# Kernel tuning notes

Measured on AMD Instinct MI355X. Metric: run time of the kernel, lower is better.

The kernel has to match this reference:

```python
import jax, jax.numpy as jnp
import numpy as np
import itertools

M_MODES = 16      # optical modes
N_PHOTONS = 8     # photons, input_state = [1]*8 + [0]*8
N_STATES = 12870  # C(16, 8) no-bunching output Fock states
OUT_SIZE = 128
BATCH = 8


def _random_unitary(key, m):
    kr, ki = jax.random.split(key)
    z = jax.random.normal(kr, (m, m)) + 1j * jax.random.normal(ki, (m, m))
    q, _ = jnp.linalg.qr(z)
    return q.astype(jnp.complex64)


def setup_inputs() -> dict:
    key = jax.random.key(0)
    ks = jax.random.split(key, 8)
    x = jax.random.normal(ks[0], (BATCH, M_MODES), dtype=jnp.float32)
    theta1 = jax.random.normal(ks[1], (M_MODES,), dtype=jnp.float32) * jnp.pi
    theta2 = jax.random.normal(ks[2], (M_MODES,), dtype=jnp.float32) * jnp.pi
    # fixed passive mixing unitaries (circuit structure constants)
    mix = jnp.stack([_random_unitary(jax.random.fold_in(ks[3], i), M_MODES) for i in range(4)])
    m_real = mix.real.astype(jnp.float32)
    m_imag = mix.imag.astype(jnp.float32)
    weight = jax.random.normal(ks[4], (N_STATES, OUT_SIZE), dtype=jnp.float32) * 0.02
    bias = jnp.zeros((OUT_SIZE,), dtype=jnp.float32)
    # no-bunching output Fock basis: all C(16,8) mode subsets (sorted rows)
    rows_idx = jnp.asarray(np.array(list(itertools.combinations(range(M_MODES), N_PHOTONS)), dtype=np.int32))
    return {"x": x, "theta1": theta1, "theta2": theta2, "m_real": m_real,
            "m_imag": m_imag, "weight": weight, "bias": bias, "rows_idx": rows_idx}


def reference(x, theta1, theta2, m_real, m_imag, weight, bias, rows_idx):
    n = N_PHOTONS
    M = (m_real + 1j * m_imag).astype(jnp.complex64)  # [4, m, m]
    # circuit unitary: U(x) = M3 . D(theta2) . M2 . D(x) . M1 . D(theta1) . M0
    A = M[1] @ (jnp.exp(1j * theta1)[:, None] * M[0])        # [m, m]
    B = M[3] @ (jnp.exp(1j * theta2)[:, None] * M[2])        # [m, m]
    U = jnp.einsum('pm,bm,mn->bpn', B, jnp.exp(1j * x), A)   # [b, m, m]
    # photons enter the first n modes -> keep those columns
    Uin = U[:, :, :n]                                        # [b, m, n]
    # Ryser's permanent formula over all 2^n column subsets
    sub = jnp.arange(2 ** n)
    masks = ((sub[:, None] >> jnp.arange(n)[None, :]) & 1).astype(jnp.float32)  # [2^n, n]
    popc = masks.sum(-1)
    signs = jnp.where((popc % 2) == 0, 1.0, -1.0) * ((-1.0) ** n)               # [2^n]
    # row partial sums for every mode and subset
    V = jnp.einsum('bmn,sn->bms', Uin, masks.astype(jnp.complex64))             # [b, m, 2^n]
    # product over the n rows of each output state (small fixed loop, not a data loop)
    acc = V[:, rows_idx[:, 0], :]                            # [b, states, 2^n]
    for i in range(1, n):
        acc = acc * V[:, rows_idx[:, i], :]
    amps = jnp.einsum('bks,s->bk', acc, signs.astype(jnp.complex64))            # [b, states]
    probs = amps.real ** 2 + amps.imag ** 2
    probs = probs / jnp.sum(probs, axis=-1, keepdims=True)   # renormalize over no-bunching subspace
    return probs @ weight + bias                             # linear output mapping
```

## Files before the change

### kernel.cpp

```cpp
#include <hip/hip_runtime.h>
#include <math.h>

#define NB 8
#define NM 16
#define NPH 8
#define NSTATES 12870
#define NSUB 256
#define OUTS 128
#define NTILES 824
#define NSLOTS (NTILES*16)
#define NSG 16
#define SPH 16
#define NTG 4
#define TILES_PER_TG 206
#define NGRID 512
#define SLOTS_P2 32
#define NP2 412

struct Tables {
  int binom[17][9];
  unsigned char cls_masks[256];
  int cls_off[10];
  int nt1[9], nt2[9];
  int tile_off[10];
};

constexpr int cpopc(int x){ int c=0; while(x){ c += x & 1; x >>= 1; } return c; }

constexpr Tables make_tables(){
  Tables t{};
  for (int n=0;n<=16;n++)
    for (int k=0;k<=8;k++){
      if (k==0) t.binom[n][k]=1;
      else if (n==0) t.binom[n][k]=0;
      else t.binom[n][k]=t.binom[n-1][k-1]+t.binom[n-1][k];
    }
  int idx=0;
  for (int p=0;p<=8;p++){
    t.cls_off[p]=idx;
    for (int m=0;m<256;m++) if (cpopc(m)==p) t.cls_masks[idx++]=(unsigned char)m;
  }
  t.cls_off[9]=idx;
  int toff=0;
  for (int c=0;c<=8;c++){
    int R=t.binom[8][c], C=t.binom[8][8-c];
    t.nt1[c]=(R+3)/4; t.nt2[c]=(C+3)/4;
    t.tile_off[c]=toff; toff += t.nt1[c]*t.nt2[c];
  }
  t.tile_off[9]=toff;
  return t;
}

constexpr Tables HTBL = make_tables();
static_assert(HTBL.tile_off[9]==NTILES, "tile count");
static_assert(HTBL.cls_off[9]==256, "mask count");
__device__ const Tables TBL = HTBL;

#define WS_TMAP   256
#define WS_BSUM2  53248
#define WS_POUT2  66560
#define WS_PART   1757184

__device__ __forceinline__ float2 cmul(float2 a, float2 b){
  return make_float2(fmaf(a.x,b.x,-(a.y*b.y)), fmaf(a.x,b.y, a.y*b.x));
}
__device__ __forceinline__ void cmac(float2& acc, float2 a, float2 b){
  acc.x = fmaf(a.x, b.x, acc.x); acc.x = fmaf(-a.y, b.y, acc.x);
  acc.y = fmaf(a.x, b.y, acc.y); acc.y = fmaf(a.y, b.x, acc.y);
}

__global__ __launch_bounds__(256) void k_p1(
    const float* __restrict__ x, const float* __restrict__ th1,
    const float* __restrict__ th2, const float* __restrict__ mr,
    const float* __restrict__ mi, const int* __restrict__ rows, char* ws)
{
  __shared__ float2 P[32][256];
  float2* __restrict__ part = (float2*)(ws + WS_PART);
  int tid = threadIdx.x;
  int blk = blockIdx.x;
  int b = blk >> 6, rest = blk & 63, sg = rest >> 2, tg = rest & 3;
  int sbase = sg * SPH;

  float2 (*T1)[NM]  = reinterpret_cast<float2(*)[NM]>(P[0]);
  float2 (*T2)[NM]  = reinterpret_cast<float2(*)[NM]>(P[1]);
  float2 (*Am)[NM]  = reinterpret_cast<float2(*)[NM]>(P[2]);
  float2 (*Bm)[NM]  = reinterpret_cast<float2(*)[NM]>(P[3]);
  float2 (*EA)[NPH] = reinterpret_cast<float2(*)[NPH]>(P[4]);
  float2* exP = P[4] + 128;
  float2 (*UinL)[NPH] = reinterpret_cast<float2(*)[NPH]>(P[5]);

  {
    int r = tid >> 4, cc = tid & 15;
    float sn, cs;
    sincosf(th1[r], &sn, &cs);
    float a = mr[0*256 + tid], bb = mi[0*256 + tid];
    T1[r][cc] = make_float2(cs*a - sn*bb, cs*bb + sn*a);
    sincosf(th2[r], &sn, &cs);
    float a2 = mr[2*256 + tid], b2 = mi[2*256 + tid];
    T2[r][cc] = make_float2(cs*a2 - sn*b2, cs*b2 + sn*a2);
    if (tid < NM){ float s2, c2; sincosf(x[b*NM + tid], &s2, &c2); exP[tid] = make_float2(c2, s2); }
  }
  __syncthreads();
  {
    int r = tid >> 4, cc = tid & 15;
    float2 accA = make_float2(0,0), accB = make_float2(0,0);
    for (int m=0;m<NM;m++){
      float2 m1 = make_float2(mr[1*256 + r*16+m], mi[1*256 + r*16+m]);
      cmac(accA, m1, T1[m][cc]);
      float2 m3 = make_float2(mr[3*256 + r*16+m], mi[3*256 + r*16+m]);
      cmac(accB, m3, T2[m][cc]);
    }
    Am[r][cc] = accA; Bm[r][cc] = accB;
  }
  __syncthreads();
  if (tid < NM*NPH){ int m = tid >> 3, n = tid & 7; EA[m][n] = cmul(exP[m], Am[m][n]); }
  __syncthreads();
  if (tid < NM*NPH){
    int p = tid >> 3, n = tid & 7;
    float2 acc = make_float2(0,0);
    for (int m=0;m<NM;m++) cmac(acc, Bm[p][m], EA[m][n]);
    UinL[p][n] = acc;
  }
  __syncthreads();

  int ts = tid >> 3;
  int table = ts >> 4, sl = ts & 15;
  int sv = sbase + sl;
  float2 v[8];
  {
    #pragma unroll
    for (int j=0;j<8;j++){
      float2 a = make_float2(0,0);
      int m = table*8 + j;
      #pragma unroll
      for (int jj=0;jj<NPH;jj++)
        if ((sv>>jj) & 1){ a.x += UinL[m][jj].x; a.y += UinL[m][jj].y; }
      v[j] = a;
    }
  }
  __syncthreads();

  {
    int chunk = tid & 7;
    int t0 = chunk << 5;
    int swz = (ts & 15) << 1;
    float2 ph = make_float2((table==0 && (__popc(sv)&1)) ? -1.0f : 1.0f, 0.0f);
    if (chunk & 4) ph = cmul(ph, v[7]);
    if (chunk & 2) ph = cmul(ph, v[6]);
    if (chunk & 1) ph = cmul(ph, v[5]);

    float2 pl[16];
    pl[0] = ph;
    #pragma unroll
    for (int w=1; w<16; w++){
      int par = w & (w-1);
      int lb = (w&1) ? 0 : ((w&2) ? 1 : ((w&4) ? 2 : 3));
      pl[w] = cmul(pl[par], v[lb]);
    }
    #pragma unroll
    for (int w=0; w<16; w+=2){
      int tc = (t0 + w) ^ swz;
      *(float4*)&P[ts][tc] = make_float4(pl[w].x, pl[w].y, pl[w+1].x, pl[w+1].y);
    }
    pl[0] = cmul(ph, v[4]);
    #pragma unroll
    for (int w=1; w<16; w++){
      int par = w & (w-1);
      int lb = (w&1) ? 0 : ((w&2) ? 1 : ((w&4) ? 2 : 3));
      pl[w] = cmul(pl[par], v[lb]);
    }
    #pragma unroll
    for (int w=0; w<16; w+=2){
      int tc = (t0 + 16 + w) ^ swz;
      *(float4*)&P[ts][tc] = make_float4(pl[w].x, pl[w].y, pl[w+1].x, pl[w+1].y);
    }
  }

  bool active = tid < TILES_PER_TG;
  int tile = tg + 4*tid;
  int t1v[4] = {0,0,0,0}, t2v[4] = {0,0,0,0};
  if (active){
    int c = 0;
    while (tile >= TBL.tile_off[c+1]) c++;
    int local = tile - TBL.tile_off[c];
    int n2 = TBL.nt2[c];
    int ti = local / n2, tj = local - ti*n2;
    int R = TBL.binom[8][c], C2 = TBL.binom[8][8-c];
    #pragma unroll
    for (int i=0;i<4;i++){ int r1 = ti*4+i; t1v[i] = (r1<R) ? (int)TBL.cls_masks[TBL.cls_off[c]+r1] : 0; }
    #pragma unroll
    for (int j=0;j<4;j++){ int r2 = tj*4+j; t2v[j] = (r2<C2) ? (int)TBL.cls_masks[TBL.cls_off[8-c]+r2] : 0; }
  }
  __syncthreads();

  if (active){
    float2 acc[4][4] = {};
    for (int s=0;s<SPH;s++){
      int swz = s << 1;
      float2 av[4], bv[4];
      #pragma unroll
      for (int i=0;i<4;i++) av[i] = P[s][t1v[i] ^ swz];
      #pragma unroll
      for (int j=0;j<4;j++) bv[j] = P[16+s][t2v[j] ^ swz];
      #pragma unroll
      for (int i=0;i<4;i++)
        #pragma unroll
        for (int j=0;j<4;j++) cmac(acc[i][j], av[i], bv[j]);
    }
    float2* dst = part + (size_t)(b*NSG + sg)*NSLOTS + (size_t)tile*16;
    #pragma unroll
    for (int i=0;i<4;i++)
      #pragma unroll
      for (int j=0;j<4;j++) dst[i*4+j] = acc[i][j];
  }

  if (tg == 3){
    int idx = blk >> 2;
    int kb = idx * 101;
    int ke = min(NSTATES, kb + 101);
    int k = kb + tid;
    if (k < ke){
      int t1=0, t2=0;
      #pragma unroll
      for (int i=0;i<NPH;i++){
        int rr = rows[k*NPH+i];
        if (rr < 8) t1 |= 1 << rr; else t2 |= 1 << (rr-8);
      }
      int c1 = __popc(t1);
      int rk1=0, cnt=0;
      #pragma unroll
      for (int bb=0;bb<8;bb++) if ((t1>>bb)&1){ cnt++; rk1 += TBL.binom[bb][cnt]; }
      int rk2=0; cnt=0;
      #pragma unroll
      for (int bb=0;bb<8;bb++) if ((t2>>bb)&1){ cnt++; rk2 += TBL.binom[bb][cnt]; }
      int tl = TBL.tile_off[c1] + (rk1>>2)*TBL.nt2[c1] + (rk2>>2);
      int slot = ((rk1&3)<<2) | (rk2&3);
      ((int*)(ws + WS_TMAP))[tl*16 + slot] = k;
    }
  }
}

__global__ __launch_bounds__(256) void k_p2(const float* __restrict__ wgt, char* ws)
{
  __shared__ float prob[NB*SLOTS_P2];
  __shared__ int   krow[SLOTS_P2];
  __shared__ float hacc[2*NB*OUTS];
  int tid = threadIdx.x;
  int blk = blockIdx.x;
  int slot0 = blk * SLOTS_P2;

  const float2* __restrict__ part = (const float2*)(ws + WS_PART);
  int bb_ = tid >> 5, sl_ = tid & 31;
  float2 vv[NSG];
  #pragma unroll
  for (int g=0; g<NSG; g++)
    vv[g] = part[(size_t)(bb_*NSG + g)*NSLOTS + slot0 + sl_];

  if (tid < SLOTS_P2){
    int slot = slot0 + tid;
    int tile = slot >> 4;
    int c = 0;
    while (tile >= TBL.tile_off[c+1]) c++;
    int local = tile - TBL.tile_off[c];
    int n2 = TBL.nt2[c];
    int ti = local / n2, tj = local - ti*n2;
    int r1 = ti*4 + ((slot >> 2) & 3);
    int r2 = tj*4 + (slot & 3);
    bool pad = (r1 >= TBL.binom[8][c]) || (r2 >= TBL.binom[8][8-c]);
    krow[tid] = pad ? -1 : ((const int*)(ws + WS_TMAP))[slot];
  }
  __syncthreads();

  float* __restrict__ bsum2 = (float*)(ws + WS_BSUM2);
  {
    float2 amp = make_float2(0,0);
    #pragma unroll
    for (int g=0; g<NSG; g++){ amp.x += vv[g].x; amp.y += vv[g].y; }
    float pr = (krow[sl_] >= 0) ? fmaf(amp.x, amp.x, amp.y*amp.y) : 0.0f;
    prob[bb_*SLOTS_P2 + sl_] = pr;
    float v = pr;
    #pragma unroll
    for (int off=16; off>0; off>>=1) v += __shfl_down(v, off, 32);
    if (sl_ == 0) bsum2[blk*NB + bb_] = v;
  }
  __syncthreads();

  {
    int h = tid >> 7, o = tid & 127;
    float acc[NB] = {0,0,0,0,0,0,0,0};
    int sbeg = h*16, send = sbeg + 16;
    #pragma unroll 4
    for (int sl = sbeg; sl < send; sl++){
      int kr = krow[sl]; if (kr < 0) kr = 0;
      float wv = wgt[(size_t)kr * OUTS + o];
      #pragma unroll
      for (int b=0;b<NB;b++) acc[b] = fmaf(prob[b*SLOTS_P2 + sl], wv, acc[b]);
    }
    #pragma unroll
    for (int b=0;b<NB;b++) hacc[h*(NB*OUTS) + b*OUTS + o] = acc[b];
  }
  __syncthreads();

  float* __restrict__ pout2 = (float*)(ws + WS_POUT2);
  for (int idx = tid; idx < NB*OUTS; idx += 256)
    pout2[(size_t)blk*(NB*OUTS) + idx] = hacc[idx] + hacc[NB*OUTS + idx];
}

__global__ __launch_bounds__(1024) void k_p3(
    const float* __restrict__ bias, const char* __restrict__ ws,
    float* __restrict__ out)
{
  __shared__ float accs[8][OUTS];
  __shared__ float wred[16];
  int tid = threadIdx.x, b = blockIdx.x;
  const float* __restrict__ bsum2 = (const float*)(ws + WS_BSUM2);
  const float* __restrict__ pout2 = (const float*)(ws + WS_POUT2);

  float v = 0.0f;
  for (int j = tid; j < NP2; j += 1024) v += bsum2[j*NB + b];
  #pragma unroll
  for (int off=32; off>0; off>>=1) v += __shfl_down(v, off);
  if ((tid & 63) == 0) wred[tid >> 6] = v;

  int o = tid & 127, grp = tid >> 7;
  float a = 0.0f;
  for (int s = grp; s < NP2; s += 8) a += pout2[(size_t)s*(NB*OUTS) + b*OUTS + o];
  accs[grp][o] = a;
  __syncthreads();
  if (tid < OUTS){
    float norm = 0.0f;
    #pragma unroll
    for (int w=0; w<16; w++) norm += wred[w];
    float r = 0.0f;
    #pragma unroll
    for (int g=0; g<8; g++) r += accs[g][tid];
    out[b*OUTS + tid] = r / norm + bias[tid];
  }
}

extern "C" void kernel_launch(void* const* d_in, const int* in_sizes, int n_in,
                              void* d_out, int out_size, void* d_ws, size_t ws_size,
                              hipStream_t stream) {
  const float* x    = (const float*)d_in[0];
  const float* th1  = (const float*)d_in[1];
  const float* th2  = (const float*)d_in[2];
  const float* mr   = (const float*)d_in[3];
  const float* mi   = (const float*)d_in[4];
  const float* wgt  = (const float*)d_in[5];
  const float* bias = (const float*)d_in[6];
  const int*   rows = (const int*)d_in[7];
  float* out = (float*)d_out;
  char* ws = (char*)d_ws;

  k_p1<<<NGRID, 256, 0, stream>>>(x, th1, th2, mr, mi, rows, ws);
  k_p2<<<NP2, 256, 0, stream>>>(wgt, ws);
  k_p3<<<NB, 1024, 0, stream>>>(bias, ws, out);
}
```

Measured before the change: 120.2 us.

## Halve k_p2 slots per block to one tile, splitting subgroup sums across thread pairs

The second-phase kernel now handles 16 slots (one tile) per block instead of 32, which doubles the grid to 824 blocks, and the workspace offsets are resized to match. Each output slot's 16 subgroup partials are split across two threads that combine through a shuffle, so every thread loads 8 values instead of 16. Tile lookup now uses the block index directly. The aim is more parallelism and memory-level concurrency in this reduction and weight-gather phase, at the cost of twice as many per-block partial outputs for the final kernel to reduce.

Result: slower. 133.8 us (+11.3%).

```diff
diff --git a/kernel.cpp b/kernel.cpp
--- a/kernel.cpp
+++ b/kernel.cpp
@@ -14,8 +14,8 @@
 #define NTG 4
 #define TILES_PER_TG 206
 #define NGRID 512
-#define SLOTS_P2 32
-#define NP2 412
+#define SLOTS_P2 16
+#define NP2 824
 
 struct Tables {
   int binom[17][9];
@@ -58,8 +58,8 @@
 
 #define WS_TMAP   256
 #define WS_BSUM2  53248
-#define WS_POUT2  66560
-#define WS_PART   1757184
+#define WS_POUT2  79872
+#define WS_PART   3455232
 
 __device__ __forceinline__ float2 cmul(float2 a, float2 b){
   return make_float2(fmaf(a.x,b.x,-(a.y*b.y)), fmaf(a.x,b.y, a.y*b.x));
@@ -250,46 +250,50 @@
   int slot0 = blk * SLOTS_P2;
 
   const float2* __restrict__ part = (const float2*)(ws + WS_PART);
-  int bb_ = tid >> 5, sl_ = tid & 31;
-  float2 vv[NSG];
+  int pidx = tid >> 1, gh = tid & 1;
+  int bb_ = pidx >> 4, sl_ = pidx & 15;
+  float2 vv[8];
   #pragma unroll
-  for (int g=0; g<NSG; g++)
-    vv[g] = part[(size_t)(bb_*NSG + g)*NSLOTS + slot0 + sl_];
+  for (int g=0; g<8; g++)
+    vv[g] = part[(size_t)(bb_*NSG + gh*8 + g)*NSLOTS + slot0 + sl_];
 
   if (tid < SLOTS_P2){
-    int slot = slot0 + tid;
-    int tile = slot >> 4;
     int c = 0;
-    while (tile >= TBL.tile_off[c+1]) c++;
-    int local = tile - TBL.tile_off[c];
+    while (blk >= TBL.tile_off[c+1]) c++;
+    int local = blk - TBL.tile_off[c];
     int n2 = TBL.nt2[c];
     int ti = local / n2, tj = local - ti*n2;
-    int r1 = ti*4 + ((slot >> 2) & 3);
-    int r2 = tj*4 + (slot & 3);
+    int r1 = ti*4 + (tid >> 2);
+    int r2 = tj*4 + (tid & 3);
     bool pad = (r1 >= TBL.binom[8][c]) || (r2 >= TBL.binom[8][8-c]);
-    krow[tid] = pad ? -1 : ((const int*)(ws + WS_TMAP))[slot];
+    krow[tid] = pad ? -1 : ((const int*)(ws + WS_TMAP))[slot0 + tid];
+  }
+  __syncthreads();
+
+  {
+    float2 amp = make_float2(0,0);
+    #pragma unroll
+    for (int g=0; g<8; g++){ amp.x += vv[g].x; amp.y += vv[g].y; }
+    amp.x += __shfl_xor(amp.x, 1);
+    amp.y += __shfl_xor(amp.y, 1);
+    float pr = (krow[sl_] >= 0) ? fmaf(amp.x, amp.x, amp.y*amp.y) : 0.0f;
+    if (gh == 0) prob[pidx] = pr;
   }
   __syncthreads();
 
   float* __restrict__ bsum2 = (float*)(ws + WS_BSUM2);
-  {
-    float2 amp = make_float2(0,0);
-    #pragma unroll
-    for (int g=0; g<NSG; g++){ amp.x += vv[g].x; amp.y += vv[g].y; }
-    float pr = (krow[sl_] >= 0) ? fmaf(amp.x, amp.x, amp.y*amp.y) : 0.0f;
-    prob[bb_*SLOTS_P2 + sl_] = pr;
-    float v = pr;
-    #pragma unroll
-    for (int off=16; off>0; off>>=1) v += __shfl_down(v, off, 32);
-    if (sl_ == 0) bsum2[blk*NB + bb_] = v;
-  }
-  __syncthreads();
+  if (tid < 128){
+    float v = prob[tid];
+    #pragma unroll
+    for (int off=8; off>0; off>>=1) v += __shfl_down(v, off, 16);
+    if ((tid & 15) == 0) bsum2[blk*NB + (tid >> 4)] = v;
+  }
 
   {
     int h = tid >> 7, o = tid & 127;
     float acc[NB] = {0,0,0,0,0,0,0,0};
-    int sbeg = h*16, send = sbeg + 16;
-    #pragma unroll 4
+    int sbeg = h*8, send = sbeg + 8;
+    #pragma unroll
     for (int sl = sbeg; sl < send; sl++){
       int kr = krow[sl]; if (kr < 0) kr = 0;
       float wv = wgt[(size_t)kr * OUTS + o];
```
